# Performance work log

Hardware: AMD Instinct MI355X
Metric: run time of the kernel (lower is better)

The kernel has to match this reference:

```python
import jax, jax.numpy as jnp
import numpy as np

B, S, D_MODEL = 4, 2048, 1024
N_HEADS, D_HEAD = 16, 64
HIDDEN = N_HEADS * D_HEAD
N_PRIM, RANK = 16, 256
CHUNK = 64  # matches CHUNK_SIZE in the torch module


def setup_inputs() -> dict:
    key = jax.random.key(0)
    ks = jax.random.split(key, 16)
    def n(k, shape, scale=0.02):
        return jax.random.normal(k, shape, dtype=jnp.float32) * scale
    return {
        'x': jax.random.normal(ks[0], (B, S, D_MODEL), dtype=jnp.float32),
        'q_U': n(ks[1], (N_PRIM, D_MODEL, RANK)),
        'q_V': n(ks[2], (N_PRIM, RANK, HIDDEN)),
        'k_U': n(ks[3], (N_PRIM, D_MODEL, RANK)),
        'k_V': n(ks[4], (N_PRIM, RANK, HIDDEN)),
        'v_U': n(ks[5], (N_PRIM, D_MODEL, RANK)),
        'v_V': n(ks[6], (N_PRIM, RANK, HIDDEN)),
        'q_logits': jax.random.normal(ks[7], (N_PRIM,), dtype=jnp.float32),
        'k_logits': jax.random.normal(ks[8], (N_PRIM,), dtype=jnp.float32),
        'v_logits': jax.random.normal(ks[9], (N_PRIM,), dtype=jnp.float32),
        'gate_logits': jax.random.normal(ks[10], (N_PRIM,), dtype=jnp.float32),
        'decay_w': n(ks[11], (N_HEADS, D_MODEL), 0.03),
        'decay_b': jnp.full((N_HEADS,), -2.0, dtype=jnp.float32),
        'out_gate_w': n(ks[12], (HIDDEN, D_MODEL), 0.03),
        'out_proj_w': n(ks[13], (D_MODEL, HIDDEN), 0.03),
        'rms_w': jnp.ones((HIDDEN,), dtype=jnp.float32),
        'top_k': 4,
    }


def _bank_topk_fused(x, U, V, logits, top_k):
    """Top-k fused mixture of low-rank primitives: sum_j w_j * (x @ U_j @ V_j)."""
    w = jax.nn.softmax(logits)                      # [P]
    vals, idx = jax.lax.top_k(w, top_k)             # [k], [k]
    vals = vals / jnp.sum(vals)                     # renormalize selected weights
    Us = U[idx]                                     # [k, d_in, rank]
    Vs = V[idx]                                     # [k, rank, d_out]
    h = jnp.einsum('bsd,kdr->bskr', x, Us)          # low-rank bottleneck
    return jnp.einsum('bskr,kro,k->bso', h, Vs, vals)


def _chunked_scan(q, kv, log_decay):
    """Decay-gated linear recurrence via chunked parallel scan (CHUNK=64).
    q, kv: [B,S,H,D]; log_decay: [B,S,H,1]. Returns [B,S,H,D]."""
    b, s, h, d = q.shape
    nc = s // CHUNK
    # [NC, B, C, H, *] chunked layout for lax.scan over chunks
    qc = jnp.moveaxis(q.reshape(b, nc, CHUNK, h, d), 1, 0)
    kvc = jnp.moveaxis(kv.reshape(b, nc, CHUNK, h, d), 1, 0)
    ldc = jnp.moveaxis(log_decay.reshape(b, nc, CHUNK, h, 1), 1, 0)

    def step(state, inp):
        ld, kvs, qs = inp                            # [B,C,H,1], [B,C,H,D], [B,C,H,D]
        cum = jnp.cumsum(ld, axis=1)                 # cumulative log-decay in chunk
        last = cum[:, -1:]
        kv_shifted = kvs * jnp.exp(last - cum)
        new = jnp.exp(cum - last) * jnp.cumsum(kv_shifted, axis=1)
        chunk_states = state[:, None] * jnp.exp(cum) + new   # [B,C,H,D]
        out = qs * chunk_states
        return chunk_states[:, -1], out

    state0 = jnp.zeros((b, h, d), dtype=jnp.float32)
    _, outs = jax.lax.scan(step, state0, (ldc, kvc, qc))     # [NC,B,C,H,D]
    return jnp.moveaxis(outs, 0, 1).reshape(b, s, h, d)


def reference(x, q_U, q_V, k_U, k_V, v_U, v_V,
              q_logits, k_logits, v_logits, gate_logits,
              decay_w, decay_b, out_gate_w, out_proj_w, rms_w, top_k):
    b, s, _ = x.shape
    h, d = decay_w.shape[0], q_V.shape[-1] // decay_w.shape[0]

    q = _bank_topk_fused(x, q_U, q_V, q_logits, top_k).reshape(b, s, h, d)
    k = _bank_topk_fused(x, k_U, k_V, k_logits, top_k).reshape(b, s, h, d)
    v = _bank_topk_fused(x, v_U, v_V, v_logits, top_k).reshape(b, s, h, d)
    # gate shares the V bank (gate = v_bank.forward_topk_fused with gate weights)
    gate = _bank_topk_fused(x, v_U, v_V, gate_logits, top_k).reshape(b, s, h, d)

    log_decay = -jax.nn.softplus(jnp.einsum('bsd,hd->bsh', x, decay_w) + decay_b)[..., None]  # [B,S,H,1]
    kv = jax.nn.sigmoid(gate) * k * v

    out = _chunked_scan(q, kv.astype(jnp.float32), log_decay.astype(jnp.float32))
    out = out.reshape(b, s, h * d)

    # RMSNorm (torch default eps = finfo.eps for fp32)
    eps = jnp.finfo(jnp.float32).eps
    out = out * jax.lax.rsqrt(jnp.mean(out * out, axis=-1, keepdims=True) + eps) * rms_w
    out = out * jax.nn.sigmoid(jnp.einsum('bsd,od->bso', x, out_gate_w))
    return jnp.einsum('bsh,dh->bsd', out, out_proj_w)
```

## Files before the change

kernel.cpp:

```cpp
#include <hip/hip_runtime.h>
#include <hip/hip_bf16.h>

#define TOK 8192
#define SEQ 2048
#define CT  32
#define NC  64

typedef __attribute__((ext_vector_type(8))) short bf16x8;
typedef __attribute__((ext_vector_type(4))) float f32x4;
typedef unsigned short u16;
typedef unsigned int   u32;

__device__ __forceinline__ u16 f2bf(float f) {
    u32 u = __float_as_uint(f);
    u = (u + 0x7FFFu + ((u >> 16) & 1u)) >> 16;
    return (u16)u;
}
__device__ __forceinline__ float b2f(u16 h) { return __uint_as_float(((u32)h) << 16); }
__device__ __forceinline__ float sigf(float z) { return 1.f / (1.f + __expf(-z)); }

__device__ __forceinline__ bf16x8 dsr128(const u16* p) {
    bf16x8 r;
    const u32 a = (u32)(size_t)(const __attribute__((address_space(3))) u16*)p;
    __asm__ volatile("ds_read_b128 %0, %1" : "=v"(r) : "v"(a));
    return r;
}

__device__ __forceinline__ void topk4(const float* __restrict__ lg, int* idx, float* wv)
{
    float v[16];
    #pragma unroll
    for (int i = 0; i < 16; i++) v[i] = lg[i];
    bool used[16];
    #pragma unroll
    for (int i = 0; i < 16; i++) used[i] = false;
    float val[4];
    #pragma unroll
    for (int k = 0; k < 4; k++) {
        int bi = 0; float bv = -3.0e38f;
        #pragma unroll
        for (int i = 0; i < 16; i++)
            if (!used[i] && v[i] > bv) { bv = v[i]; bi = i; }
        used[bi] = true; idx[k] = bi; val[k] = bv;
    }
    float e[4], s = 0.f;
    #pragma unroll
    for (int k = 0; k < 4; k++) { e[k] = expf(val[k] - val[0]); s += e[k]; }
    #pragma unroll
    for (int k = 0; k < 4; k++) wv[k] = e[k] / s;
}

__global__ __launch_bounds__(256)
void prep(const float* __restrict__ x, const float* __restrict__ ogw,
          const float* __restrict__ opw,
          const float* __restrict__ qU, const float* __restrict__ kU,
          const float* __restrict__ vU,
          const float* __restrict__ qV, const float* __restrict__ kV,
          const float* __restrict__ vV,
          const float* __restrict__ ql, const float* __restrict__ kl,
          const float* __restrict__ vl, const float* __restrict__ gl,
          const float* __restrict__ dw, const float* __restrict__ db,
          u16* __restrict__ xb, u16* __restrict__ ogwb, u16* __restrict__ opwb,
          u16* __restrict__ gU, u16* __restrict__ gVT, float* __restrict__ dec)
{
    const int blk = blockIdx.x;
    const int tid = threadIdx.x;

    if (blk < 2048) {
        const int wave = tid >> 6, lane = tid & 63;
        const int t = blk * 4 + wave;
        const float4* x4 = (const float4*)(x + (size_t)t * 1024);
        float4 xv[4];
        #pragma unroll
        for (int i = 0; i < 4; i++) xv[i] = x4[lane + 64 * i];
        uint2* xrow = (uint2*)(xb + (size_t)t * 1024);
        #pragma unroll
        for (int i = 0; i < 4; i++) {
            __align__(8) u16 tq[4] = { f2bf(xv[i].x), f2bf(xv[i].y),
                                       f2bf(xv[i].z), f2bf(xv[i].w) };
            xrow[lane + 64 * i] = *(const uint2*)tq;
        }
        float p[16];
        #pragma unroll
        for (int h = 0; h < 16; h++) {
            const float4* w4 = (const float4*)(dw + (size_t)h * 1024);
            float s = 0.f;
            #pragma unroll
            for (int i = 0; i < 4; i++) {
                const float4 wv = w4[lane + 64 * i];
                s = fmaf(xv[i].x, wv.x, fmaf(xv[i].y, wv.y,
                    fmaf(xv[i].z, wv.z, fmaf(xv[i].w, wv.w, s))));
            }
            p[h] = s;
        }
        #pragma unroll
        for (int off = 32; off > 0; off >>= 1)
            #pragma unroll
            for (int h = 0; h < 16; h++) p[h] += __shfl_xor(p[h], off);
        if (lane == 0) {
            #pragma unroll
            for (int h = 0; h < 16; h++)
                dec[(size_t)t * 16 + h] = 1.f / (1.f + __expf(p[h] + db[h]));
        }
        return;
    }
    if (blk < 4096) {
        const float* src; u16* dst;
        int off;
        if (blk < 3072) { src = ogw; dst = ogwb; off = (blk - 2048) * 256 + tid; }
        else            { src = opw; dst = opwb; off = (blk - 3072) * 256 + tid; }
        const float4 v = ((const float4*)src)[off];
        __align__(8) u16 t[4] = { f2bf(v.x), f2bf(v.y), f2bf(v.z), f2bf(v.w) };
        ((uint2*)dst)[off] = *(const uint2*)t;
        return;
    }
    {
        const int local = blk - 4096;
        const int z = local >> 8;
        const int bx = local & 15, by = (local >> 4) & 15;
        const int p = z & 3;
        const float* lg = (p == 0) ? ql : (p == 1) ? kl : (p == 2) ? vl : gl;
        int idx[4]; float wsel[4];
        topk4(lg, idx, wsel);

        if (z < 4) {
            const float* V = (p == 0) ? qV : (p == 1) ? kV : vV;
            const int o0 = bx * 64, k0 = by * 64;
            const int s = k0 >> 8, r0 = k0 & 255;
            const float* Vb = V + (size_t)idx[s] * (256 * 1024);
            __shared__ float tile[64][68];
            const int rr = tid >> 4, cc = (tid & 15) << 2;
            #pragma unroll
            for (int i = 0; i < 4; i++) {
                const float4 v = *(const float4*)(Vb + (size_t)(r0 + rr + 16 * i) * 1024 + o0 + cc);
                *(float4*)&tile[rr + 16 * i][cc] = v;
            }
            __syncthreads();
            const int oo = tid >> 4, kk = (tid & 15) << 2;
            u16* out = gVT + (size_t)p * 1048576;
            #pragma unroll
            for (int i = 0; i < 4; i++) {
                __align__(8) u16 t[4];
                #pragma unroll
                for (int j = 0; j < 4; j++) t[j] = f2bf(tile[kk + j][oo + 16 * i]);
                *(uint2*)(out + (size_t)(o0 + oo + 16 * i) * 1024 + k0 + kk) = *(const uint2*)t;
            }
        } else {
            const float* U = (p == 0) ? qU : (p == 1) ? kU : vU;
            const int d0 = bx * 64, k0 = by * 64;
            const int s = k0 >> 8, r0 = k0 & 255;
            const float* Ub = U + (size_t)idx[s] * (1024 * 256);
            const float wq = wsel[s];
            u16* out = gU + (size_t)p * 1048576;
            const int rr = tid >> 4, cc = (tid & 15) << 2;
            #pragma unroll
            for (int i = 0; i < 4; i++) {
                const float4 v = *(const float4*)(Ub + (size_t)(d0 + rr + 16 * i) * 256 + r0 + cc);
                __align__(8) u16 t[4] = { f2bf(v.x * wq), f2bf(v.y * wq),
                                          f2bf(v.z * wq), f2bf(v.w * wq) };
                *(uint2*)(out + (size_t)(d0 + rr + 16 * i) * 1024 + k0 + cc) = *(const uint2*)t;
            }
        }
    }
}

__global__ __launch_bounds__(256)
void mfma_gemm64(const u16* __restrict__ Asrc, const u16* __restrict__ Bsrc,
                 u16* __restrict__ Cout)
{
    __shared__ u16 As[64 * 64];
    __shared__ u16 Bs[64 * 64];
    const int z = blockIdx.z;
    const u16* A = Asrc + (size_t)z * 1048576;
    const u16* B = Bsrc + (size_t)z * 1048576;
    u16* C = Cout + (size_t)z * 1048576;
    const int tid = threadIdx.x, lane = tid & 63, wave = tid >> 6;
    const int m0 = blockIdx.y * 64, n0 = blockIdx.x * 64;
    const int wn = wave * 16;

    f32x4 acc[4];
    #pragma unroll
    for (int i = 0; i < 4; i++) acc[i] = (f32x4)0.f;

    for (int k0 = 0; k0 < 1024; k0 += 64) {
        __syncthreads();
        #pragma unroll
        for (int it = 0; it < 2; it++) {
            const int c   = it * 256 + tid;
            const int row = c >> 3, j = c & 7;
            const int g   = j ^ (row & 7);
            const u16* ga = A + (size_t)(m0 + row) * 1024 + k0 + g * 8;
            __builtin_amdgcn_global_load_lds(
                (const __attribute__((address_space(1))) u32*)ga,
                (__attribute__((address_space(3))) u32*)&As[(it * 256 + wave * 64) * 8],
                16, 0, 0);
            const u16* gb = B + (size_t)(n0 + row) * 1024 + k0 + g * 8;
            __builtin_amdgcn_global_load_lds(
                (const __attribute__((address_space(1))) u32*)gb,
                (__attribute__((address_space(3))) u32*)&Bs[(it * 256 + wave * 64) * 8],
                16, 0, 0);
        }
        __syncthreads();
        #pragma unroll
        for (int ks = 0; ks < 2; ks++) {
            const int gk = ks * 4 + (lane >> 4);
            const int rn = wn + (lane & 15);
            const int jb = gk ^ (rn & 7);
            const bf16x8 bfr = *(const bf16x8*)&Bs[rn * 64 + jb * 8];
            #pragma unroll
            for (int mi = 0; mi < 4; mi++) {
                const int rm = mi * 16 + (lane & 15);
                const int ja = gk ^ (rm & 7);
                const bf16x8 af = *(const bf16x8*)&As[rm * 64 + ja * 8];
                acc[mi] = __builtin_amdgcn_mfma_f32_16x16x32_bf16(af, bfr, acc[mi], 0, 0, 0);
            }
        }
    }
    const int col_l = lane & 15, row_l = (lane >> 4) * 4;
    #pragma unroll
    for (int mi = 0; mi < 4; mi++)
        #pragma unroll
        for (int i = 0; i < 4; i++)
            C[(size_t)(m0 + mi * 16 + row_l + i) * 1024 + n0 + wn + col_l] = f2bf(acc[mi][i]);
}

__global__ __launch_bounds__(512)
void mfma_gemm256(const u16* __restrict__ Asrc, const u16* __restrict__ Bt,
                  u16* __restrict__ Cout)
{
    __shared__ __align__(16) u16 Alds[2][2][8192];
    __shared__ __align__(16) u16 Blds[2][2][8192];

    const int flat  = blockIdx.x;
    const int xcd   = flat & 7;
    const int local = flat >> 3;
    const int zb    = local >> 4;
    const int rem   = local & 15;
    const int m0    = (xcd * 4 + (rem >> 2)) * 256;
    const int n0    = (rem & 3) * 256;

    const u16* A = Asrc;
    const u16* B = Bt + (size_t)zb * 1048576;
    u16*       C = Cout + (size_t)zb * 8388608;

    const int tid  = threadIdx.x;
    const int lane = tid & 63, wave = tid >> 6;
    const int wmi  = wave >> 2, wni = wave & 3;
    const int l15  = lane & 15, l4 = lane >> 4;

    f32x4 acc[8][4];
    #pragma unroll
    for (int i = 0; i < 8; i++)
        #pragma unroll
        for (int j = 0; j < 4; j++) acc[i][j] = (f32x4)0.f;

    bf16x8 a_fr[2][4];
    bf16x8 b_fr[2][2][2];

#define STAGE_A(BUFP, HALF, T) do {                                           \
    _Pragma("unroll")                                                         \
    for (int it_ = 0; it_ < 2; it_++) {                                       \
        const int bc_ = it_ * 512 + wave * 64;                                \
        const int c_  = bc_ + lane;                                           \
        const int r_  = c_ >> 3, j_ = c_ & 7;                                 \
        const int g_  = j_ ^ (r_ & 7);                                        \
        const int gr_ = m0 + ((r_ >> 6) << 7) + (HALF) * 64 + (r_ & 63);      \
        const u16* ga_ = A + (size_t)gr_ * 1024 + (T) * 64 + g_ * 8;          \
        __builtin_amdgcn_global_load_lds(                                     \
            (const __attribute__((address_space(1))) u32*)ga_,                \
            (__attribute__((address_space(3))) u32*)&(BUFP)[(HALF)][bc_ * 8], \
            16, 0, 0);                                                        \
    } } while (0)

#define STAGE_B(BUFP, HALF, T) do {                                           \
    _Pragma("unroll")                                                         \
    for (int it_ = 0; it_ < 2; it_++) {                                       \
        const int bc_ = it_ * 512 + wave * 64;                                \
        const int c_  = bc_ + lane;                                           \
        const int r_  = c_ >> 3, j_ = c_ & 7;                                 \
        const int g_  = j_ ^ (r_ & 7);                                        \
        const int gr_ = n0 + ((r_ >> 5) << 6) + (HALF) * 32 + (r_ & 31);      \
        const u16* gb_ = B + (size_t)gr_ * 1024 + (T) * 64 + g_ * 8;          \
        __builtin_amdgcn_global_load_lds(                                     \
            (const __attribute__((address_space(1))) u32*)gb_,                \
            (__attribute__((address_space(3))) u32*)&(BUFP)[(HALF)][bc_ * 8], \
            16, 0, 0);                                                        \
    } } while (0)

#define READ_A(BUFP, QM) do {                                                 \
    _Pragma("unroll") for (int ks_ = 0; ks_ < 2; ks_++)                       \
    _Pragma("unroll") for (int m4_ = 0; m4_ < 4; m4_++) {                     \
        const int r_  = wmi * 64 + m4_ * 16 + l15;                            \
        const int gk_ = ks_ * 4 + l4;                                         \
        a_fr[ks_][m4_] =                                                      \
            dsr128(&(BUFP)[QM][r_ * 64 + ((gk_ ^ (r_ & 7)) * 8)]);            \
    } } while (0)

#define READ_B(BUFP, QN) do {                                                 \
    _Pragma("unroll") for (int ks_ = 0; ks_ < 2; ks_++)                       \
    _Pragma("unroll") for (int n2_ = 0; n2_ < 2; n2_++) {                     \
        const int r_  = wni * 32 + n2_ * 16 + l15;                            \
        const int gk_ = ks_ * 4 + l4;                                         \
        b_fr[QN][ks_][n2_] =                                                  \
            dsr128(&(BUFP)[QN][r_ * 64 + ((gk_ ^ (r_ & 7)) * 8)]);            \
    } } while (0)

#define MFMA_PH(QM, QN) do {                                                  \
    __builtin_amdgcn_s_setprio(1);                                            \
    _Pragma("unroll") for (int ks_ = 0; ks_ < 2; ks_++)                       \
    _Pragma("unroll") for (int m4_ = 0; m4_ < 4; m4_++)                       \
    _Pragma("unroll") for (int n2_ = 0; n2_ < 2; n2_++)                       \
        acc[(QM) * 4 + m4_][(QN) * 2 + n2_] =                                 \
            __builtin_amdgcn_mfma_f32_16x16x32_bf16(                          \
                a_fr[ks_][m4_], b_fr[QN][ks_][n2_],                           \
                acc[(QM) * 4 + m4_][(QN) * 2 + n2_], 0, 0, 0);                \
    __builtin_amdgcn_s_setprio(0);                                            \
} while (0)

#define BAR()    __builtin_amdgcn_s_barrier()
#define LGKM0()  do { __asm__ volatile("s_waitcnt lgkmcnt(0)");               \
                      __builtin_amdgcn_sched_barrier(0); } while (0)
#define VMCNT8() do { __asm__ volatile("s_waitcnt vmcnt(8)");                 \
                      __builtin_amdgcn_sched_barrier(0); } while (0)
#define VMCNT4() do { __asm__ volatile("s_waitcnt vmcnt(4)");                 \
                      __builtin_amdgcn_sched_barrier(0); } while (0)
#define VMCNT0() do { __asm__ volatile("s_waitcnt vmcnt(0)");                 \
                      __builtin_amdgcn_sched_barrier(0); } while (0)

    STAGE_A(Alds[0], 0, 0);
    STAGE_B(Blds[0], 0, 0);
    STAGE_A(Alds[0], 1, 0);
    STAGE_B(Blds[0], 1, 0);
    STAGE_A(Alds[1], 0, 1);
    STAGE_B(Blds[1], 0, 1);
    VMCNT8(); BAR();

    #pragma unroll 1
    for (int t = 0; t < 16; ++t) {
        const int b = t & 1, nb = b ^ 1;
        u16 (*Ab)[8192] = Alds[b];
        u16 (*Bb)[8192] = Blds[b];

        READ_A(Ab, 0);
        READ_B(Bb, 0);
        if (t + 1 < 16) { STAGE_A(Alds[nb], 1, t + 1); STAGE_B(Blds[nb], 1, t + 1); }
        BAR();
        LGKM0();
        MFMA_PH(0, 0);
        if (t < 15) { VMCNT8(); } else { VMCNT0(); }
        BAR();

        READ_B(Bb, 1);
        if (t + 2 < 16) STAGE_A(Alds[b], 0, t + 2);
        BAR();
        LGKM0();
        MFMA_PH(0, 1);
        BAR();

        READ_A(Ab, 1);
        BAR();
        LGKM0();
        MFMA_PH(1, 0);
        BAR();

        if (t + 2 < 16) STAGE_B(Blds[b], 0, t + 2);
        BAR();
        MFMA_PH(1, 1);
        if (t + 2 < 16)      { VMCNT8(); }
        else if (t + 1 < 16) { VMCNT4(); }
        BAR();
    }

#undef STAGE_A
#undef STAGE_B
#undef READ_A
#undef READ_B
#undef MFMA_PH
#undef BAR
#undef LGKM0
#undef VMCNT8
#undef VMCNT4
#undef VMCNT0

    const int col_l = lane & 15, row_l = (lane >> 4) * 4;
    #pragma unroll
    for (int mi = 0; mi < 8; mi++)
        #pragma unroll
        for (int ni = 0; ni < 4; ni++)
            #pragma unroll
            for (int i = 0; i < 4; i++) {
                const int rw = m0 + wmi * 128 + mi * 16 + row_l + i;
                const int cn = n0 + wni * 64 + ni * 16 + col_l;
                C[(size_t)rw * 1024 + cn] = f2bf(acc[mi][ni][i]);
            }
}

template<int OUTBF>
__global__ __launch_bounds__(256)
void mfma_gemm(const u16* __restrict__ Asrc, const u16* __restrict__ Bt,
               void* __restrict__ Cout, size_t astride, size_t bstride, size_t cstride)
{
    __shared__ u16 As[128 * 64];
    __shared__ u16 Bs[128 * 64];
    const int flat = blockIdx.x + 8 * (blockIdx.y + 64 * blockIdx.z);
    const int xcd = flat & 7;
    const int r   = flat >> 3;
    const int nb = r & 7, mlocal = (r >> 3) & 7, zb = r >> 6;
    const int m0 = (xcd * 8 + mlocal) * 128, n0 = nb * 128;

    const u16* A = Asrc + (size_t)zb * astride;
    const u16* B = Bt   + (size_t)zb * bstride;
    const int tid  = threadIdx.x;
    const int lane = tid & 63, wave = tid >> 6;
    const int wm = (wave >> 1) * 64, wn = (wave & 1) * 64;

    f32x4 acc[4][4];
    #pragma unroll
    for (int i = 0; i < 4; i++)
        #pragma unroll
        for (int j = 0; j < 4; j++) acc[i][j] = (f32x4)0.f;

    for (int k0 = 0; k0 < 1024; k0 += 64) {
        __syncthreads();
        #pragma unroll
        for (int it = 0; it < 4; it++) {
            const int c   = it * 256 + tid;
            const int row = c >> 3, j = c & 7;
            const int g   = j ^ (row & 7);
            const u16* ga = A + (size_t)(m0 + row) * 1024 + k0 + g * 8;
            __builtin_amdgcn_global_load_lds(
                (const __attribute__((address_space(1))) u32*)ga,
                (__attribute__((address_space(3))) u32*)&As[(it * 256 + wave * 64) * 8],
                16, 0, 0);
            const u16* gb = B + (size_t)(n0 + row) * 1024 + k0 + g * 8;
            __builtin_amdgcn_global_load_lds(
                (const __attribute__((address_space(1))) u32*)gb,
                (__attribute__((address_space(3))) u32*)&Bs[(it * 256 + wave * 64) * 8],
                16, 0, 0);
        }
        __syncthreads();
        #pragma unroll
        for (int ks = 0; ks < 2; ks++) {
            bf16x8 af[4], bfr[4];
            const int gk = ks * 4 + (lane >> 4);
            #pragma unroll
            for (int mi = 0; mi < 4; mi++) {
                const int rr  = wm + mi * 16 + (lane & 15);
                const int ja = gk ^ (rr & 7);
                af[mi] = *(const bf16x8*)&As[rr * 64 + ja * 8];
                const int rn = wn + mi * 16 + (lane & 15);
                const int jb = gk ^ (rn & 7);
                bfr[mi] = *(const bf16x8*)&Bs[rn * 64 + jb * 8];
            }
            #pragma unroll
            for (int mi = 0; mi < 4; mi++)
                #pragma unroll
                for (int ni = 0; ni < 4; ni++)
                    acc[mi][ni] = __builtin_amdgcn_mfma_f32_16x16x32_bf16(
                        af[mi], bfr[ni], acc[mi][ni], 0, 0, 0);
        }
    }
    const int col_l = lane & 15, row_l = (lane >> 4) * 4;
    if (OUTBF) {
        u16* C = (u16*)Cout + (size_t)zb * cstride;
        #pragma unroll
        for (int mi = 0; mi < 4; mi++)
            #pragma unroll
            for (int ni = 0; ni < 4; ni++)
                #pragma unroll
                for (int i = 0; i < 4; i++) {
                    const int rw  = m0 + wm + mi * 16 + row_l + i;
                    const int cn = n0 + wn + ni * 16 + col_l;
                    C[(size_t)rw * 1024 + cn] = f2bf(acc[mi][ni][i]);
                }
    } else {
        float* C = (float*)Cout + (size_t)zb * cstride;
        #pragma unroll
        for (int mi = 0; mi < 4; mi++)
            #pragma unroll
            for (int ni = 0; ni < 4; ni++)
                #pragma unroll
                for (int i = 0; i < 4; i++) {
                    const int rw  = m0 + wm + mi * 16 + row_l + i;
                    const int cn = n0 + wn + ni * 16 + col_l;
                    C[(size_t)rw * 1024 + cn] = acc[mi][ni][i];
                }
    }
}

__global__ __launch_bounds__(256)
void scan1(const u16* __restrict__ Kq, const u16* __restrict__ Vq, const u16* __restrict__ Gq,
           const float* __restrict__ dec, u16* __restrict__ kvb,
           float* __restrict__ Lc, float* __restrict__ Pc)
{
    const int unit = blockIdx.x * 4 + (threadIdx.x >> 6);
    const int d = threadIdx.x & 63;
    const int c = unit & (NC - 1), h = (unit >> 6) & 15, b = unit >> 10;
    const size_t t0 = (size_t)b * SEQ + c * CT;
    const size_t base = t0 * 1024 + h * 64 + d;
    const u16* kp = Kq + base;
    const u16* vp = Vq + base;
    const u16* gp = Gq + base;
    const float* dp = dec + t0 * 16 + h;
    float s = 0.f, P = 1.f;
    #pragma unroll 4
    for (int t = 0; t < CT; t++) {
        const size_t o = (size_t)t * 1024;
        const float a  = dp[t * 16];
        const u16 kq = f2bf(b2f(kp[o]) * b2f(vp[o]) * sigf(b2f(gp[o])));
        kvb[base + o] = kq;
        s = fmaf(a, s, b2f(kq));
        P *= a;
    }
    const int ci = (b * 16 + h) * NC + c;
    Lc[(size_t)ci * 64 + d] = s;
    if (d == 0) Pc[ci] = P;
}

__global__ __launch_bounds__(256)
void scan3(const u16* __restrict__ Qq, const u16* __restrict__ kvb,
           const float* __restrict__ dec,
           const float* __restrict__ Lc, const float* __restrict__ Pc,
           u16* __restrict__ attb)
{
    const int unit = blockIdx.x * 4 + (threadIdx.x >> 6);
    const int d = threadIdx.x & 63;
    const int c = unit & (NC - 1), h = (unit >> 6) & 15, b = unit >> 10;
    const size_t t0 = (size_t)b * SEQ + c * CT;
    const size_t base = t0 * 1024 + h * 64 + d;
    const u16* qp = Qq + base;
    const u16* kp = kvb + base;
    const float* dp = dec + t0 * 16 + h;

    const int ci0 = (b * 16 + h) * NC;
    float s = 0.f;
    for (int cc = 0; cc < c; cc++)
        s = fmaf(Pc[ci0 + cc], s, Lc[(size_t)(ci0 + cc) * 64 + d]);

    #pragma unroll 4
    for (int t = 0; t < CT; t++) {
        const size_t o = (size_t)t * 1024;
        const float a  = dp[t * 16];
        s = fmaf(a, s, b2f(kp[o]));
        attb[base + o] = f2bf(b2f(qp[o]) * s);
    }
}

__global__ __launch_bounds__(256)
void rms_gate(const u16* __restrict__ attb, const u16* __restrict__ gpre,
              const float* __restrict__ rmsw, u16* __restrict__ o)
{
    const int wave = threadIdx.x >> 6, lane = threadIdx.x & 63;
    const size_t t = (size_t)blockIdx.x * 4 + wave;
    const ushort4* ap = (const ushort4*)(attb + t * 1024);
    ushort4 a4[4];
    float ss = 0.f;
    #pragma unroll
    for (int i = 0; i < 4; i++) {
        a4[i] = ap[lane + 64 * i];
        const float ax = b2f(a4[i].x), ay = b2f(a4[i].y);
        const float az = b2f(a4[i].z), aw = b2f(a4[i].w);
        ss += ax*ax + ay*ay + az*az + aw*aw;
    }
    #pragma unroll
    for (int off = 32; off > 0; off >>= 1) ss += __shfl_xor(ss, off);
    const float scale = rsqrtf(ss * (1.0f / 1024.0f) + 1.1920929e-7f);
    const ushort4* gp = (const ushort4*)(gpre + t * 1024);
    const float4*  wp = (const float4*)rmsw;
    uint2* op = (uint2*)(o + t * 1024);
    #pragma unroll
    for (int i = 0; i < 4; i++) {
        const ushort4 g4 = gp[lane + 64 * i];
        const float4  w  = wp[lane + 64 * i];
        __align__(8) u16 r[4];
        r[0] = f2bf(b2f(a4[i].x) * scale * w.x * sigf(b2f(g4.x)));
        r[1] = f2bf(b2f(a4[i].y) * scale * w.y * sigf(b2f(g4.y)));
        r[2] = f2bf(b2f(a4[i].z) * scale * w.z * sigf(b2f(g4.z)));
        r[3] = f2bf(b2f(a4[i].w) * scale * w.w * sigf(b2f(g4.w)));
        op[lane + 64 * i] = *(const uint2*)r;
    }
}

extern "C" void kernel_launch(void* const* d_in, const int* in_sizes, int n_in,
                              void* d_out, int out_size, void* d_ws, size_t ws_size,
                              hipStream_t stream)
{
    const float* x    = (const float*)d_in[0];
    const float* qU   = (const float*)d_in[1];
    const float* qV   = (const float*)d_in[2];
    const float* kU   = (const float*)d_in[3];
    const float* kV   = (const float*)d_in[4];
    const float* vU   = (const float*)d_in[5];
    const float* vV   = (const float*)d_in[6];
    const float* ql   = (const float*)d_in[7];
    const float* kl   = (const float*)d_in[8];
    const float* vl   = (const float*)d_in[9];
    const float* gl   = (const float*)d_in[10];
    const float* dw   = (const float*)d_in[11];
    const float* db   = (const float*)d_in[12];
    const float* ogw  = (const float*)d_in[13];
    const float* opw  = (const float*)d_in[14];
    const float* rmsw = (const float*)d_in[15];

    char* w = (char*)d_ws;
    float* dec  = (float*)(w + 0);
    u16*   WT   = (u16*)  (w + 524288);
    u16*   xb   = (u16*)  (w + 11010048);
    u16*   opwb = (u16*)  (w + 27787264);
    u16*   QKVG = (u16*)  (w + 29884416);
    u16*   RMSO = (u16*)  (w + 113770496);
    u16*   ATTb = (u16*)  (w + 130547712);
    u16*   kvb  = (u16*)  (w + 147324928);
    float* Lc   = (float*)(w + 164102144);
    float* Pc   = (float*)(w + 165150720);
    u16*   gU   = QKVG;
    u16*   gVT  = QKVG + 4194304;
    u16*   ogwb = WT + 4 * 1048576;
    u16*   GPRE = QKVG + 4 * 8388608;

    prep<<<6144, 256, 0, stream>>>(x, ogw, opw, qU, kU, vU, qV, kV, vV,
                                   ql, kl, vl, gl, dw, db,
                                   xb, ogwb, opwb, gU, gVT, dec);

    mfma_gemm64<<<dim3(16, 16, 4), 256, 0, stream>>>(gVT, gU, WT);

    mfma_gemm256<<<640, 512, 0, stream>>>(xb, WT, QKVG);

    scan1<<<1024, 256, 0, stream>>>(QKVG + 8388608, QKVG + 16777216, QKVG + 25165824,
                                    dec, kvb, Lc, Pc);
    scan3<<<1024, 256, 0, stream>>>(QKVG, kvb, dec, Lc, Pc, ATTb);

    rms_gate<<<2048, 256, 0, stream>>>(ATTb, GPRE, rmsw, RMSO);

    mfma_gemm<0><<<dim3(8, 64, 1), 256, 0, stream>>>(RMSO, opwb, (float*)d_out, 0, 0, 0);
}
```

Measured before the change: 390.5 us.

## Enlarge weight-fusion GEMM tiles to 128x128 and vectorize scan kernels by four

The weight-product GEMM moves from 64x64 tiles, where each wave computed a 64x16 strip, to 128x128 tiles where each wave computes a 64x64 block with 4x4 MFMA accumulators. This raises fragment reuse from LDS and cuts global traffic per FLOP. The two scan kernels now give each thread four adjacent head dims, using 8-byte vector loads and stores, and launch a quarter as many blocks. The trade-offs are higher register pressure in the GEMM, fewer blocks in flight for the smaller launches (256 blocks for each scan), and more serial work per thread.

```diff
diff --git a/kernel.cpp b/kernel.cpp
--- a/kernel.cpp
+++ b/kernel.cpp
@@ -165,27 +165,30 @@
 }
 
 __global__ __launch_bounds__(256)
-void mfma_gemm64(const u16* __restrict__ Asrc, const u16* __restrict__ Bsrc,
-                 u16* __restrict__ Cout)
-{
-    __shared__ u16 As[64 * 64];
-    __shared__ u16 Bs[64 * 64];
+void mfma_gemm128w(const u16* __restrict__ Asrc, const u16* __restrict__ Bsrc,
+                   u16* __restrict__ Cout)
+{
+    __shared__ u16 As[128 * 64];
+    __shared__ u16 Bs[128 * 64];
     const int z = blockIdx.z;
     const u16* A = Asrc + (size_t)z * 1048576;
     const u16* B = Bsrc + (size_t)z * 1048576;
     u16* C = Cout + (size_t)z * 1048576;
-    const int tid = threadIdx.x, lane = tid & 63, wave = tid >> 6;
-    const int m0 = blockIdx.y * 64, n0 = blockIdx.x * 64;
-    const int wn = wave * 16;
-
-    f32x4 acc[4];
-    #pragma unroll
-    for (int i = 0; i < 4; i++) acc[i] = (f32x4)0.f;
+    const int tid  = threadIdx.x;
+    const int lane = tid & 63, wave = tid >> 6;
+    const int m0 = blockIdx.y * 128, n0 = blockIdx.x * 128;
+    const int wm = (wave >> 1) * 64, wn = (wave & 1) * 64;
+
+    f32x4 acc[4][4];
+    #pragma unroll
+    for (int i = 0; i < 4; i++)
+        #pragma unroll
+        for (int j = 0; j < 4; j++) acc[i][j] = (f32x4)0.f;
 
     for (int k0 = 0; k0 < 1024; k0 += 64) {
         __syncthreads();
         #pragma unroll
-        for (int it = 0; it < 2; it++) {
+        for (int it = 0; it < 4; it++) {
             const int c   = it * 256 + tid;
             const int row = c >> 3, j = c & 7;
             const int g   = j ^ (row & 7);
@@ -203,25 +206,36 @@
         __syncthreads();
         #pragma unroll
         for (int ks = 0; ks < 2; ks++) {
+            bf16x8 af[4], bfr[4];
             const int gk = ks * 4 + (lane >> 4);
-            const int rn = wn + (lane & 15);
-            const int jb = gk ^ (rn & 7);
-            const bf16x8 bfr = *(const bf16x8*)&Bs[rn * 64 + jb * 8];
             #pragma unroll
             for (int mi = 0; mi < 4; mi++) {
-                const int rm = mi * 16 + (lane & 15);
-                const int ja = gk ^ (rm & 7);
-                const bf16x8 af = *(const bf16x8*)&As[rm * 64 + ja * 8];
-                acc[mi] = __builtin_amdgcn_mfma_f32_16x16x32_bf16(af, bfr, acc[mi], 0, 0, 0);
-            }
+                const int rr  = wm + mi * 16 + (lane & 15);
+                const int ja = gk ^ (rr & 7);
+                af[mi] = *(const bf16x8*)&As[rr * 64 + ja * 8];
+                const int rn = wn + mi * 16 + (lane & 15);
+                const int jb = gk ^ (rn & 7);
+                bfr[mi] = *(const bf16x8*)&Bs[rn * 64 + jb * 8];
+            }
+            #pragma unroll
+            for (int mi = 0; mi < 4; mi++)
+                #pragma unroll
+                for (int ni = 0; ni < 4; ni++)
+                    acc[mi][ni] = __builtin_amdgcn_mfma_f32_16x16x32_bf16(
+                        af[mi], bfr[ni], acc[mi][ni], 0, 0, 0);
         }
     }
     const int col_l = lane & 15, row_l = (lane >> 4) * 4;
     #pragma unroll
     for (int mi = 0; mi < 4; mi++)
         #pragma unroll
-        for (int i = 0; i < 4; i++)
-            C[(size_t)(m0 + mi * 16 + row_l + i) * 1024 + n0 + wn + col_l] = f2bf(acc[mi][i]);
+        for (int ni = 0; ni < 4; ni++)
+            #pragma unroll
+            for (int i = 0; i < 4; i++) {
+                const int rw = m0 + wm + mi * 16 + row_l + i;
+                const int cn = n0 + wn + ni * 16 + col_l;
+                C[(size_t)rw * 1024 + cn] = f2bf(acc[mi][ni][i]);
+            }
 }
 
 __global__ __launch_bounds__(512)
@@ -494,27 +508,38 @@
            float* __restrict__ Lc, float* __restrict__ Pc)
 {
     const int unit = blockIdx.x * 4 + (threadIdx.x >> 6);
-    const int d = threadIdx.x & 63;
-    const int c = unit & (NC - 1), h = (unit >> 6) & 15, b = unit >> 10;
+    const int l = threadIdx.x & 63;
+    const int c = unit & (NC - 1), hg = (unit >> 6) & 3, b = unit >> 8;
+    const int h  = hg * 4 + (l >> 4);
+    const int d0 = (l & 15) * 4;
     const size_t t0 = (size_t)b * SEQ + c * CT;
-    const size_t base = t0 * 1024 + h * 64 + d;
-    const u16* kp = Kq + base;
-    const u16* vp = Vq + base;
-    const u16* gp = Gq + base;
+    const size_t base = t0 * 1024 + (size_t)h * 64 + d0;
     const float* dp = dec + t0 * 16 + h;
-    float s = 0.f, P = 1.f;
-    #pragma unroll 4
+
+    float4 s = {0.f, 0.f, 0.f, 0.f};
+    float P = 1.f;
+    #pragma unroll 8
     for (int t = 0; t < CT; t++) {
-        const size_t o = (size_t)t * 1024;
-        const float a  = dp[t * 16];
-        const u16 kq = f2bf(b2f(kp[o]) * b2f(vp[o]) * sigf(b2f(gp[o])));
-        kvb[base + o] = kq;
-        s = fmaf(a, s, b2f(kq));
+        const size_t o = base + (size_t)t * 1024;
+        const float a = dp[t * 16];
+        const ushort4 k4 = *(const ushort4*)(Kq + o);
+        const ushort4 v4 = *(const ushort4*)(Vq + o);
+        const ushort4 g4 = *(const ushort4*)(Gq + o);
+        __align__(8) u16 kq[4];
+        kq[0] = f2bf(b2f(k4.x) * b2f(v4.x) * sigf(b2f(g4.x)));
+        kq[1] = f2bf(b2f(k4.y) * b2f(v4.y) * sigf(b2f(g4.y)));
+        kq[2] = f2bf(b2f(k4.z) * b2f(v4.z) * sigf(b2f(g4.z)));
+        kq[3] = f2bf(b2f(k4.w) * b2f(v4.w) * sigf(b2f(g4.w)));
+        *(uint2*)(kvb + o) = *(const uint2*)kq;
+        s.x = fmaf(a, s.x, b2f(kq[0]));
+        s.y = fmaf(a, s.y, b2f(kq[1]));
+        s.z = fmaf(a, s.z, b2f(kq[2]));
+        s.w = fmaf(a, s.w, b2f(kq[3]));
         P *= a;
     }
     const int ci = (b * 16 + h) * NC + c;
-    Lc[(size_t)ci * 64 + d] = s;
-    if (d == 0) Pc[ci] = P;
+    *(float4*)(Lc + (size_t)ci * 64 + d0) = s;
+    if ((l & 15) == 0) Pc[ci] = P;
 }
 
 __global__ __launch_bounds__(256)
@@ -524,25 +549,41 @@
            u16* __restrict__ attb)
 {
     const int unit = blockIdx.x * 4 + (threadIdx.x >> 6);
-    const int d = threadIdx.x & 63;
-    const int c = unit & (NC - 1), h = (unit >> 6) & 15, b = unit >> 10;
+    const int l = threadIdx.x & 63;
+    const int c = unit & (NC - 1), hg = (unit >> 6) & 3, b = unit >> 8;
+    const int h  = hg * 4 + (l >> 4);
+    const int d0 = (l & 15) * 4;
     const size_t t0 = (size_t)b * SEQ + c * CT;
-    const size_t base = t0 * 1024 + h * 64 + d;
-    const u16* qp = Qq + base;
-    const u16* kp = kvb + base;
+    const size_t base = t0 * 1024 + (size_t)h * 64 + d0;
     const float* dp = dec + t0 * 16 + h;
 
     const int ci0 = (b * 16 + h) * NC;
-    float s = 0.f;
-    for (int cc = 0; cc < c; cc++)
-        s = fmaf(Pc[ci0 + cc], s, Lc[(size_t)(ci0 + cc) * 64 + d]);
-
-    #pragma unroll 4
+    float4 s = {0.f, 0.f, 0.f, 0.f};
+    for (int cc = 0; cc < c; cc++) {
+        const float p = Pc[ci0 + cc];
+        const float4 L = *(const float4*)(Lc + (size_t)(ci0 + cc) * 64 + d0);
+        s.x = fmaf(p, s.x, L.x);
+        s.y = fmaf(p, s.y, L.y);
+        s.z = fmaf(p, s.z, L.z);
+        s.w = fmaf(p, s.w, L.w);
+    }
+
+    #pragma unroll 8
     for (int t = 0; t < CT; t++) {
-        const size_t o = (size_t)t * 1024;
-        const float a  = dp[t * 16];
-        s = fmaf(a, s, b2f(kp[o]));
-        attb[base + o] = f2bf(b2f(qp[o]) * s);
+        const size_t o = base + (size_t)t * 1024;
+        const float a = dp[t * 16];
+        const ushort4 q4 = *(const ushort4*)(Qq + o);
+        const ushort4 k4 = *(const ushort4*)(kvb + o);
+        s.x = fmaf(a, s.x, b2f(k4.x));
+        s.y = fmaf(a, s.y, b2f(k4.y));
+        s.z = fmaf(a, s.z, b2f(k4.z));
+        s.w = fmaf(a, s.w, b2f(k4.w));
+        __align__(8) u16 r[4];
+        r[0] = f2bf(b2f(q4.x) * s.x);
+        r[1] = f2bf(b2f(q4.y) * s.y);
+        r[2] = f2bf(b2f(q4.z) * s.z);
+        r[3] = f2bf(b2f(q4.w) * s.w);
+        *(uint2*)(attb + o) = *(const uint2*)r;
     }
 }
 
@@ -622,13 +663,13 @@
                                    ql, kl, vl, gl, dw, db,
                                    xb, ogwb, opwb, gU, gVT, dec);
 
-    mfma_gemm64<<<dim3(16, 16, 4), 256, 0, stream>>>(gVT, gU, WT);
+    mfma_gemm128w<<<dim3(8, 8, 4), 256, 0, stream>>>(gVT, gU, WT);
 
     mfma_gemm256<<<640, 512, 0, stream>>>(xb, WT, QKVG);
 
-    scan1<<<1024, 256, 0, stream>>>(QKVG + 8388608, QKVG + 16777216, QKVG + 25165824,
-                                    dec, kvb, Lc, Pc);
-    scan3<<<1024, 256, 0, stream>>>(QKVG, kvb, dec, Lc, Pc, ATTb);
+    scan1<<<256, 256, 0, stream>>>(QKVG + 8388608, QKVG + 16777216, QKVG + 25165824,
+                                   dec, kvb, Lc, Pc);
+    scan3<<<256, 256, 0, stream>>>(QKVG, kvb, dec, Lc, Pc, ATTb);
 
     rms_gate<<<2048, 256, 0, stream>>>(ATTb, GPRE, rmsw, RMSO);
 
```

Result: slower. 411.7 us (+5.4%).

## Fuse scan3 with RMSNorm gating and enlarge weight-fold GEMM tile to 128x128

Applied to the files above, without the earlier changes.

Merges the second scan pass with the RMSNorm and output-gate kernel. Each 1024-thread block covers all 16 heads of one 32-token chunk, reduces per-token squared norms through shared memory, and writes the gated result directly, so the bf16 attention intermediate is never written to or read back from global memory. Separately, the U·V weight-fold GEMM moves from 64x64 tiles with a 4-MFMA-per-wave inner loop to 128x128 tiles with a 4x4 MFMA block per wave, for more reuse per LDS load. The trade-offs are fewer, larger blocks (256 blocks for the scan) and higher register pressure from holding 32 per-token values and 16 accumulators.

```diff
diff --git a/kernel.cpp b/kernel.cpp
--- a/kernel.cpp
+++ b/kernel.cpp
@@ -165,27 +165,30 @@
 }
 
 __global__ __launch_bounds__(256)
-void mfma_gemm64(const u16* __restrict__ Asrc, const u16* __restrict__ Bsrc,
-                 u16* __restrict__ Cout)
-{
-    __shared__ u16 As[64 * 64];
-    __shared__ u16 Bs[64 * 64];
+void mfma_gemm128w(const u16* __restrict__ Asrc, const u16* __restrict__ Bsrc,
+                   u16* __restrict__ Cout)
+{
+    __shared__ u16 As[128 * 64];
+    __shared__ u16 Bs[128 * 64];
     const int z = blockIdx.z;
     const u16* A = Asrc + (size_t)z * 1048576;
     const u16* B = Bsrc + (size_t)z * 1048576;
     u16* C = Cout + (size_t)z * 1048576;
-    const int tid = threadIdx.x, lane = tid & 63, wave = tid >> 6;
-    const int m0 = blockIdx.y * 64, n0 = blockIdx.x * 64;
-    const int wn = wave * 16;
-
-    f32x4 acc[4];
-    #pragma unroll
-    for (int i = 0; i < 4; i++) acc[i] = (f32x4)0.f;
+    const int tid  = threadIdx.x;
+    const int lane = tid & 63, wave = tid >> 6;
+    const int m0 = blockIdx.y * 128, n0 = blockIdx.x * 128;
+    const int wm = (wave >> 1) * 64, wn = (wave & 1) * 64;
+
+    f32x4 acc[4][4];
+    #pragma unroll
+    for (int i = 0; i < 4; i++)
+        #pragma unroll
+        for (int j = 0; j < 4; j++) acc[i][j] = (f32x4)0.f;
 
     for (int k0 = 0; k0 < 1024; k0 += 64) {
         __syncthreads();
         #pragma unroll
-        for (int it = 0; it < 2; it++) {
+        for (int it = 0; it < 4; it++) {
             const int c   = it * 256 + tid;
             const int row = c >> 3, j = c & 7;
             const int g   = j ^ (row & 7);
@@ -203,25 +206,36 @@
         __syncthreads();
         #pragma unroll
         for (int ks = 0; ks < 2; ks++) {
+            bf16x8 af[4], bfr[4];
             const int gk = ks * 4 + (lane >> 4);
-            const int rn = wn + (lane & 15);
-            const int jb = gk ^ (rn & 7);
-            const bf16x8 bfr = *(const bf16x8*)&Bs[rn * 64 + jb * 8];
             #pragma unroll
             for (int mi = 0; mi < 4; mi++) {
-                const int rm = mi * 16 + (lane & 15);
-                const int ja = gk ^ (rm & 7);
-                const bf16x8 af = *(const bf16x8*)&As[rm * 64 + ja * 8];
-                acc[mi] = __builtin_amdgcn_mfma_f32_16x16x32_bf16(af, bfr, acc[mi], 0, 0, 0);
-            }
+                const int rr  = wm + mi * 16 + (lane & 15);
+                const int ja = gk ^ (rr & 7);
+                af[mi] = *(const bf16x8*)&As[rr * 64 + ja * 8];
+                const int rn = wn + mi * 16 + (lane & 15);
+                const int jb = gk ^ (rn & 7);
+                bfr[mi] = *(const bf16x8*)&Bs[rn * 64 + jb * 8];
+            }
+            #pragma unroll
+            for (int mi = 0; mi < 4; mi++)
+                #pragma unroll
+                for (int ni = 0; ni < 4; ni++)
+                    acc[mi][ni] = __builtin_amdgcn_mfma_f32_16x16x32_bf16(
+                        af[mi], bfr[ni], acc[mi][ni], 0, 0, 0);
         }
     }
     const int col_l = lane & 15, row_l = (lane >> 4) * 4;
     #pragma unroll
     for (int mi = 0; mi < 4; mi++)
         #pragma unroll
-        for (int i = 0; i < 4; i++)
-            C[(size_t)(m0 + mi * 16 + row_l + i) * 1024 + n0 + wn + col_l] = f2bf(acc[mi][i]);
+        for (int ni = 0; ni < 4; ni++)
+            #pragma unroll
+            for (int i = 0; i < 4; i++) {
+                const int rw = m0 + wm + mi * 16 + row_l + i;
+                const int cn = n0 + wn + ni * 16 + col_l;
+                C[(size_t)rw * 1024 + cn] = f2bf(acc[mi][ni][i]);
+            }
 }
 
 __global__ __launch_bounds__(512)
@@ -497,7 +511,7 @@
     const int d = threadIdx.x & 63;
     const int c = unit & (NC - 1), h = (unit >> 6) & 15, b = unit >> 10;
     const size_t t0 = (size_t)b * SEQ + c * CT;
-    const size_t base = t0 * 1024 + h * 64 + d;
+    const size_t base = t0 * 1024 + (size_t)h * 64 + d;
     const u16* kp = Kq + base;
     const u16* vp = Vq + base;
     const u16* gp = Gq + base;
@@ -517,17 +531,20 @@
     if (d == 0) Pc[ci] = P;
 }
 
-__global__ __launch_bounds__(256)
-void scan3(const u16* __restrict__ Qq, const u16* __restrict__ kvb,
-           const float* __restrict__ dec,
-           const float* __restrict__ Lc, const float* __restrict__ Pc,
-           u16* __restrict__ attb)
-{
-    const int unit = blockIdx.x * 4 + (threadIdx.x >> 6);
-    const int d = threadIdx.x & 63;
-    const int c = unit & (NC - 1), h = (unit >> 6) & 15, b = unit >> 10;
+__global__ __launch_bounds__(1024)
+void scan3_rms(const u16* __restrict__ Qq, const u16* __restrict__ kvb,
+               const float* __restrict__ dec,
+               const float* __restrict__ Lc, const float* __restrict__ Pc,
+               const u16* __restrict__ gpre, const float* __restrict__ rmsw,
+               u16* __restrict__ o)
+{
+    __shared__ float ssq[16][32];
+    __shared__ float sscale[32];
+
+    const int b = blockIdx.x >> 6, c = blockIdx.x & 63;
+    const int h = threadIdx.x >> 6, d = threadIdx.x & 63;
     const size_t t0 = (size_t)b * SEQ + c * CT;
-    const size_t base = t0 * 1024 + h * 64 + d;
+    const size_t base = t0 * 1024 + (size_t)h * 64 + d;
     const u16* qp = Qq + base;
     const u16* kp = kvb + base;
     const float* dp = dec + t0 * 16 + h;
@@ -537,47 +554,39 @@
     for (int cc = 0; cc < c; cc++)
         s = fmaf(Pc[ci0 + cc], s, Lc[(size_t)(ci0 + cc) * 64 + d]);
 
-    #pragma unroll 4
+    float av[CT];
+    #pragma unroll
     for (int t = 0; t < CT; t++) {
-        const size_t o = (size_t)t * 1024;
-        const float a  = dp[t * 16];
-        s = fmaf(a, s, b2f(kp[o]));
-        attb[base + o] = f2bf(b2f(qp[o]) * s);
-    }
-}
-
-__global__ __launch_bounds__(256)
-void rms_gate(const u16* __restrict__ attb, const u16* __restrict__ gpre,
-              const float* __restrict__ rmsw, u16* __restrict__ o)
-{
-    const int wave = threadIdx.x >> 6, lane = threadIdx.x & 63;
-    const size_t t = (size_t)blockIdx.x * 4 + wave;
-    const ushort4* ap = (const ushort4*)(attb + t * 1024);
-    ushort4 a4[4];
-    float ss = 0.f;
-    #pragma unroll
-    for (int i = 0; i < 4; i++) {
-        a4[i] = ap[lane + 64 * i];
-        const float ax = b2f(a4[i].x), ay = b2f(a4[i].y);
-        const float az = b2f(a4[i].z), aw = b2f(a4[i].w);
-        ss += ax*ax + ay*ay + az*az + aw*aw;
-    }
-    #pragma unroll
-    for (int off = 32; off > 0; off >>= 1) ss += __shfl_xor(ss, off);
-    const float scale = rsqrtf(ss * (1.0f / 1024.0f) + 1.1920929e-7f);
-    const ushort4* gp = (const ushort4*)(gpre + t * 1024);
-    const float4*  wp = (const float4*)rmsw;
-    uint2* op = (uint2*)(o + t * 1024);
-    #pragma unroll
-    for (int i = 0; i < 4; i++) {
-        const ushort4 g4 = gp[lane + 64 * i];
-        const float4  w  = wp[lane + 64 * i];
-        __align__(8) u16 r[4];
-        r[0] = f2bf(b2f(a4[i].x) * scale * w.x * sigf(b2f(g4.x)));
-        r[1] = f2bf(b2f(a4[i].y) * scale * w.y * sigf(b2f(g4.y)));
-        r[2] = f2bf(b2f(a4[i].z) * scale * w.z * sigf(b2f(g4.z)));
-        r[3] = f2bf(b2f(a4[i].w) * scale * w.w * sigf(b2f(g4.w)));
-        op[lane + 64 * i] = *(const uint2*)r;
+        const size_t oo = (size_t)t * 1024;
+        const float a = dp[t * 16];
+        s = fmaf(a, s, b2f(kp[oo]));
+        av[t] = b2f(f2bf(b2f(qp[oo]) * s));
+    }
+
+    #pragma unroll
+    for (int t = 0; t < CT; t++) {
+        float p = av[t] * av[t];
+        #pragma unroll
+        for (int off = 32; off > 0; off >>= 1) p += __shfl_xor(p, off);
+        if (d == 0) ssq[h][t] = p;
+    }
+    __syncthreads();
+
+    if (threadIdx.x < 32) {
+        const int t = threadIdx.x;
+        float tot = 0.f;
+        #pragma unroll
+        for (int hh = 0; hh < 16; hh++) tot += ssq[hh][t];
+        sscale[t] = rsqrtf(tot * (1.0f / 1024.0f) + 1.1920929e-7f);
+    }
+    __syncthreads();
+
+    const float w = rmsw[h * 64 + d];
+    #pragma unroll
+    for (int t = 0; t < CT; t++) {
+        const size_t oo = (size_t)t * 1024;
+        const float g = b2f(gpre[base + oo]);
+        o[base + oo] = f2bf(av[t] * sscale[t] * w * sigf(g));
     }
 }
 
@@ -609,7 +618,6 @@
     u16*   opwb = (u16*)  (w + 27787264);
     u16*   QKVG = (u16*)  (w + 29884416);
     u16*   RMSO = (u16*)  (w + 113770496);
-    u16*   ATTb = (u16*)  (w + 130547712);
     u16*   kvb  = (u16*)  (w + 147324928);
     float* Lc   = (float*)(w + 164102144);
     float* Pc   = (float*)(w + 165150720);
@@ -622,15 +630,14 @@
                                    ql, kl, vl, gl, dw, db,
                                    xb, ogwb, opwb, gU, gVT, dec);
 
-    mfma_gemm64<<<dim3(16, 16, 4), 256, 0, stream>>>(gVT, gU, WT);
+    mfma_gemm128w<<<dim3(8, 8, 4), 256, 0, stream>>>(gVT, gU, WT);
 
     mfma_gemm256<<<640, 512, 0, stream>>>(xb, WT, QKVG);
 
     scan1<<<1024, 256, 0, stream>>>(QKVG + 8388608, QKVG + 16777216, QKVG + 25165824,
                                     dec, kvb, Lc, Pc);
-    scan3<<<1024, 256, 0, stream>>>(QKVG, kvb, dec, Lc, Pc, ATTb);
-
-    rms_gate<<<2048, 256, 0, stream>>>(ATTb, GPRE, rmsw, RMSO);
+
+    scan3_rms<<<256, 1024, 0, stream>>>(QKVG, kvb, dec, Lc, Pc, GPRE, rmsw, RMSO);
 
     mfma_gemm<0><<<dim3(8, 64, 1), 256, 0, stream>>>(RMSO, opwb, (float*)d_out, 0, 0, 0);
 }
```

After: 398.1 us. Within noise of the previous version (+1.9%).
